# Performance work log

Hardware: AMD Instinct MI355X
Metric: run time of the kernel (lower is better)

Reference implementation:

```python
import jax, jax.numpy as jnp
import numpy as np


def setup_inputs() -> dict:
    key = jax.random.key(0)
    kq, kk, kv = jax.random.split(key, 3)
    B, H, T, D = 2, 8, 8192, 64
    return {
        "Q": jax.random.normal(kq, (B, H, T, D), dtype=jnp.float32),
        "K": jax.random.normal(kk, (B, H, T, D), dtype=jnp.float32),
        "V": jax.random.normal(kv, (B, H, T, D), dtype=jnp.float32),
        "window_size": 512,
    }


def _gather_bands(x, nb, Wn):
    # x: [B,H,T,D] -> [B,H,nb,3*Wn,D], key blocks (i-1, i, i+1) per query block i
    B, H, T, D = x.shape
    xb = x.reshape(B, H, nb, Wn, D)
    xp = jnp.pad(xb, ((0, 0), (0, 0), (1, 1), (0, 0), (0, 0)))
    return jnp.concatenate([xp[:, :, i:i + nb] for i in range(3)], axis=3)


def reference(Q, K, V, window_size):
    # Sliding-window attention: softmax over keys with |q_idx - kv_idx| <= window_size,
    # computed block-sparsely (only the 3 neighboring key blocks per query block).
    B, H, T, D = Q.shape
    Wn = int(window_size)
    assert T % Wn == 0
    nb = T // Wn
    scale = 1.0 / (D ** 0.5)

    Qb = Q.reshape(B, H, nb, Wn, D)
    Kw = _gather_bands(K, nb, Wn)  # [B,H,nb,3W,D]
    Vw = _gather_bands(V, nb, Wn)

    # scores within the band: [B,H,nb,W,3W]
    s = jnp.einsum('bhnqd,bhnkd->bhnqk', Qb, Kw) * scale

    # exact band mask: global q = n*W + q_loc, global kv = (n-1)*W + k_loc
    q_loc = jnp.arange(Wn)[:, None]
    k_loc = jnp.arange(3 * Wn)[None, :]
    band = jnp.abs(q_loc + Wn - k_loc) <= Wn          # [W, 3W]
    kv_g = (jnp.arange(nb)[:, None] - 1) * Wn + jnp.arange(3 * Wn)[None, :]  # [nb, 3W]
    valid = (kv_g >= 0) & (kv_g < T)
    mask = band[None, :, :] & valid[:, None, :]        # [nb, W, 3W]

    s = jnp.where(mask[None, None], s, -jnp.inf)
    p = jax.nn.softmax(s, axis=-1)
    o = jnp.einsum('bhnqk,bhnkd->bhnqd', p, Vw)
    return o.reshape(B, H, T, D)
```

## Files before the change

### kernel.cpp

```cpp
#include <hip/hip_runtime.h>
#include <hip/hip_bf16.h>
#include <stdint.h>

typedef __attribute__((ext_vector_type(8))) short bf16x8;
typedef __attribute__((ext_vector_type(4))) short bf16x4;
typedef __attribute__((ext_vector_type(4))) float f32x4;

#define T_SEQ   8192
#define D_HEAD  64
#define NHEADS  16
#define WIN     512
#define BQ      128
#define BK      64
#define NTILES  (T_SEQ / BK)
#define LDSR    72
#define MASKVAL (-1.0e6f)

#define WS_NEEDED ((size_t)2 * NHEADS * T_SEQ * D_HEAD * 2)

#define MFMA16(a,b,c) __builtin_amdgcn_mfma_f32_16x16x16bf16_1k(a,b,c,0,0,0)

extern "C" __device__ __attribute__((const)) float __ocml_native_exp2_f32(float);
__device__ __forceinline__ float fexp2(float x) { return __ocml_native_exp2_f32(x); }

__device__ __forceinline__ short f2bf(float f) {
    union { float f; uint32_t u; } v; v.f = f;
    return (short)((v.u + 0x7FFFu + ((v.u >> 16) & 1u)) >> 16);
}

__device__ __forceinline__ uint32_t pkbf2(float lo, float hi) {
    union { __hip_bfloat162 h; uint32_t u; } c;
    c.h = __float22bfloat162_rn(make_float2(lo, hi));
    return c.u;
}

__global__ __launch_bounds__(256, 2)
void prep_kv(const float* __restrict__ Kg, const float* __restrict__ Vg,
             short* __restrict__ Kb, short* __restrict__ Vt)
{
    __shared__ float vt[64 * 65];
    const int tid  = threadIdx.x;
    const int tile = blockIdx.x & (NTILES - 1);
    const int head = blockIdx.x >> 7;
    const size_t off = ((size_t)head * T_SEQ + (size_t)tile * BK) * D_HEAD;

    const float* ks = Kg + off;
    short* kd = Kb + off;
    #pragma unroll
    for (int i = 0; i < 4; ++i) {
        int idx = tid + 256 * i;
        float4 v = *(const float4*)(ks + idx * 4);
        short4 h = { f2bf(v.x), f2bf(v.y), f2bf(v.z), f2bf(v.w) };
        *(short4*)(kd + idx * 4) = h;
    }

    const float* vs = Vg + off;
    #pragma unroll
    for (int i = 0; i < 4; ++i) {
        int idx = tid + 256 * i;
        int row = idx >> 4, c4 = (idx & 15) << 2;
        float4 v = *(const float4*)(vs + row * D_HEAD + c4);
        *(float4*)&vt[row * 65 + c4] = v;
    }
    __syncthreads();
    short* vd = Vt + ((size_t)head * NTILES + tile) * (BK * D_HEAD);
    {
        int d = tid >> 2, kq = (tid & 3) << 4;
        short out[16];
        #pragma unroll
        for (int j = 0; j < 16; ++j) out[j] = f2bf(vt[(kq + j) * 65 + d]);
        *(bf16x8*)(vd + d * BK + kq)     = *(bf16x8*)&out[0];
        *(bf16x8*)(vd + d * BK + kq + 8) = *(bf16x8*)&out[8];
    }
}

__global__ __launch_bounds__(256, 4)
void swa_fwd(const float* __restrict__ Qg, const short* __restrict__ Kb,
             const short* __restrict__ Vt, float* __restrict__ Og)
{
    __shared__ short Ks[BK * LDSR];
    __shared__ short Vs[D_HEAD * LDSR];

    const int tid  = threadIdx.x;
    const int wave = tid >> 6;
    const int lane = tid & 63;
    const int lcol = lane & 15;
    const int quad = lane >> 4;

    const int g    = blockIdx.x;
    const int head = (g >> 3) >> 3;
    const int qt   = ((g & 7) << 3) | ((g >> 3) & 7);
    const int q0   = qt * BQ;
    const int tq   = q0 >> 6;

    const float* Qp = Qg + (size_t)head * T_SEQ * D_HEAD;
    const short* Kp = Kb + (size_t)head * T_SEQ * D_HEAD;
    float*       Op = Og + (size_t)head * T_SEQ * D_HEAD;

    const float qscale = 0.125f * 1.44269504088896340736f;
    const int qrow_w = q0 + wave * 32;

    bf16x8 qf[2][2];
    #pragma unroll
    for (int mt = 0; mt < 2; ++mt) {
        const float* qptr = Qp + (size_t)(qrow_w + mt*16 + lcol) * D_HEAD + quad * 8;
        #pragma unroll
        for (int ks = 0; ks < 2; ++ks) {
            float4 a = *(const float4*)(qptr + ks*32);
            float4 b = *(const float4*)(qptr + ks*32 + 4);
            bf16x8 f;
            f[0]=f2bf(a.x*qscale); f[1]=f2bf(a.y*qscale); f[2]=f2bf(a.z*qscale); f[3]=f2bf(a.w*qscale);
            f[4]=f2bf(b.x*qscale); f[5]=f2bf(b.y*qscale); f[6]=f2bf(b.z*qscale); f[7]=f2bf(b.w*qscale);
            qf[mt][ks] = f;
        }
    }

    f32x4 oacc[2][4];
    float l_run[2];
    const f32x4 zero4 = {0.f, 0.f, 0.f, 0.f};
    #pragma unroll
    for (int mt = 0; mt < 2; ++mt) {
        l_run[mt] = 0.f;
        #pragma unroll
        for (int nt = 0; nt < 4; ++nt) oacc[mt][nt] = zero4;
    }

    int t0 = (q0 - WIN) >> 6;            if (t0 < 0) t0 = 0;
    int t1 = (q0 + BQ - 1 + WIN) >> 6;   if (t1 > NTILES - 1) t1 = NTILES - 1;

    const int srow0 = tid >> 3, sc0 = (tid & 7) << 3;
    const int srow1 = srow0 + 32;

    for (int t = t0; t <= t1; ++t) {
        const short* ksrc = Kp + (size_t)t * BK * D_HEAD;
        const short* vsrc = Vt + ((size_t)head * NTILES + t) * (BK * D_HEAD);
        bf16x8 k0 = *(const bf16x8*)(ksrc + tid * 8);
        bf16x8 k1 = *(const bf16x8*)(ksrc + (tid + 256) * 8);
        bf16x8 v0 = *(const bf16x8*)(vsrc + tid * 8);
        bf16x8 v1 = *(const bf16x8*)(vsrc + (tid + 256) * 8);

        __syncthreads();

        *(bf16x8*)&Ks[srow0 * LDSR + sc0] = k0;
        *(bf16x8*)&Ks[srow1 * LDSR + sc0] = k1;
        *(bf16x8*)&Vs[srow0 * LDSR + sc0] = v0;
        *(bf16x8*)&Vs[srow1 * LDSR + sc0] = v1;

        __syncthreads();

        const bool edge = (t < tq - 6) || (t > tq + 7);

        #pragma unroll
        for (int h = 0; h < 2; ++h) {
            f32x4 sc[2][2];
            #pragma unroll
            for (int j = 0; j < 2; ++j) { sc[j][0] = zero4; sc[j][1] = zero4; }
            #pragma unroll
            for (int ks = 0; ks < 2; ++ks) {
                #pragma unroll
                for (int j = 0; j < 2; ++j) {
                    bf16x8 kf = *(const bf16x8*)&Ks[((2*h+j)*16 + lcol)*LDSR + ks*32 + quad*8];
                    sc[j][0] = __builtin_amdgcn_mfma_f32_16x16x32_bf16(kf, qf[0][ks], sc[j][0], 0,0,0);
                    sc[j][1] = __builtin_amdgcn_mfma_f32_16x16x32_bf16(kf, qf[1][ks], sc[j][1], 0,0,0);
                }
            }

            if (edge) {
                #pragma unroll
                for (int j = 0; j < 2; ++j) {
                    const int kg0 = t*BK + (2*h+j)*16 + quad*4;
                    #pragma unroll
                    for (int mt = 0; mt < 2; ++mt) {
                        const int qg = qrow_w + mt*16 + lcol;
                        #pragma unroll
                        for (int r = 0; r < 4; ++r) {
                            int dq = qg - (kg0 + r);
                            if (dq > WIN || dq < -WIN) sc[j][mt][r] = MASKVAL;
                        }
                    }
                }
            }

            #pragma unroll
            for (int j = 0; j < 2; ++j) {
                const int kt = 2*h + j;
                bf16x4 vf[4];
                #pragma unroll
                for (int nt = 0; nt < 4; ++nt)
                    vf[nt] = *(const bf16x4*)&Vs[(nt*16 + lcol)*LDSR + kt*16 + quad*4];
                #pragma unroll
                for (int mt = 0; mt < 2; ++mt) {
                    float p0 = fexp2(sc[j][mt][0]);
                    float p1 = fexp2(sc[j][mt][1]);
                    float p2 = fexp2(sc[j][mt][2]);
                    float p3 = fexp2(sc[j][mt][3]);
                    l_run[mt] += (p0 + p1) + (p2 + p3);
                    union { int2 i; bf16x4 v; } pf;
                    pf.i = make_int2((int)pkbf2(p0, p1), (int)pkbf2(p2, p3));
                    #pragma unroll
                    for (int nt = 0; nt < 4; ++nt)
                        oacc[mt][nt] = MFMA16(vf[nt], pf.v, oacc[mt][nt]);
                }
            }
        }
    }

    #pragma unroll
    for (int mt = 0; mt < 2; ++mt) {
        float l = l_run[mt];
        l += __shfl_xor(l, 16, 64);
        l += __shfl_xor(l, 32, 64);
        float inv = 1.0f / l;
        const int qg = qrow_w + mt*16 + lcol;
        float* op = Op + (size_t)qg * D_HEAD + quad*4;
        #pragma unroll
        for (int nt = 0; nt < 4; ++nt) {
            float4 o = { oacc[mt][nt][0]*inv, oacc[mt][nt][1]*inv,
                         oacc[mt][nt][2]*inv, oacc[mt][nt][3]*inv };
            *(float4*)(op + nt*16) = o;
        }
    }
}

__global__ __launch_bounds__(256, 4)
void swa_fused_fb(const float* __restrict__ Qg, const float* __restrict__ Kg,
                  const float* __restrict__ Vg, float* __restrict__ Og)
{
    __shared__ short Ks[BK * LDSR];
    __shared__ short Vs[D_HEAD * LDSR];
    __shared__ float Vtmp[BK * 65];

    const int tid  = threadIdx.x;
    const int wave = tid >> 6;
    const int lane = tid & 63;
    const int lcol = lane & 15;
    const int quad = lane >> 4;

    const int g    = blockIdx.x;
    const int head = g >> 6;
    const int qt   = ((g & 7) << 3) | ((g >> 3) & 7);
    const int q0   = qt * BQ;
    const int tq   = q0 >> 6;

    const size_t hoff = (size_t)head * T_SEQ * D_HEAD;
    const float* Qp = Qg + hoff;
    const float* Kp = Kg + hoff;
    const float* Vp = Vg + hoff;
    float*       Op = Og + hoff;

    const float qscale = 0.125f * 1.44269504088896340736f;
    const int qrow_w = q0 + wave * 32;

    bf16x8 qf[2][2];
    #pragma unroll
    for (int mt = 0; mt < 2; ++mt) {
        const float* qptr = Qp + (size_t)(qrow_w + mt*16 + lcol) * D_HEAD + quad * 8;
        #pragma unroll
        for (int ks = 0; ks < 2; ++ks) {
            float4 a = *(const float4*)(qptr + ks*32);
            float4 b = *(const float4*)(qptr + ks*32 + 4);
            bf16x8 f;
            f[0]=f2bf(a.x*qscale); f[1]=f2bf(a.y*qscale); f[2]=f2bf(a.z*qscale); f[3]=f2bf(a.w*qscale);
            f[4]=f2bf(b.x*qscale); f[5]=f2bf(b.y*qscale); f[6]=f2bf(b.z*qscale); f[7]=f2bf(b.w*qscale);
            qf[mt][ks] = f;
        }
    }

    f32x4 oacc[2][4];
    float l_run[2];
    const f32x4 zero4 = {0.f, 0.f, 0.f, 0.f};
    #pragma unroll
    for (int mt = 0; mt < 2; ++mt) {
        l_run[mt] = 0.f;
        #pragma unroll
        for (int nt = 0; nt < 4; ++nt) oacc[mt][nt] = zero4;
    }

    int t0 = (q0 - WIN) >> 6;            if (t0 < 0) t0 = 0;
    int t1 = (q0 + BQ - 1 + WIN) >> 6;   if (t1 > NTILES - 1) t1 = NTILES - 1;

    const int krow0 = tid >> 3, kc = (tid & 7) << 3;
    const int krow1 = krow0 + 32;
    const int vrow  = tid >> 4, vc = (tid & 15) << 2;
    const int td    = tid >> 2, tkq = (tid & 3) << 4;

    for (int t = t0; t <= t1; ++t) {
        const float* ksrc = Kp + (size_t)t * BK * D_HEAD;
        const float* vsrc = Vp + (size_t)t * BK * D_HEAD;
        float4 k00 = *(const float4*)(ksrc + krow0*D_HEAD + kc);
        float4 k01 = *(const float4*)(ksrc + krow0*D_HEAD + kc + 4);
        float4 k10 = *(const float4*)(ksrc + krow1*D_HEAD + kc);
        float4 k11 = *(const float4*)(ksrc + krow1*D_HEAD + kc + 4);
        float4 v0  = *(const float4*)(vsrc + (vrow     )*D_HEAD + vc);
        float4 v1  = *(const float4*)(vsrc + (vrow + 16)*D_HEAD + vc);
        float4 v2  = *(const float4*)(vsrc + (vrow + 32)*D_HEAD + vc);
        float4 v3  = *(const float4*)(vsrc + (vrow + 48)*D_HEAD + vc);

        __syncthreads();

        *(float4*)&Vtmp[(vrow     )*65 + vc] = v0;
        *(float4*)&Vtmp[(vrow + 16)*65 + vc] = v1;
        *(float4*)&Vtmp[(vrow + 32)*65 + vc] = v2;
        *(float4*)&Vtmp[(vrow + 48)*65 + vc] = v3;
        *(int4*)&Ks[krow0*LDSR + kc] = make_int4((int)pkbf2(k00.x,k00.y), (int)pkbf2(k00.z,k00.w),
                                                 (int)pkbf2(k01.x,k01.y), (int)pkbf2(k01.z,k01.w));
        *(int4*)&Ks[krow1*LDSR + kc] = make_int4((int)pkbf2(k10.x,k10.y), (int)pkbf2(k10.z,k10.w),
                                                 (int)pkbf2(k11.x,k11.y), (int)pkbf2(k11.z,k11.w));

        __syncthreads();

        {
            uint32_t w0 = pkbf2(Vtmp[(tkq+ 0)*65 + td], Vtmp[(tkq+ 1)*65 + td]);
            uint32_t w1 = pkbf2(Vtmp[(tkq+ 2)*65 + td], Vtmp[(tkq+ 3)*65 + td]);
            uint32_t w2 = pkbf2(Vtmp[(tkq+ 4)*65 + td], Vtmp[(tkq+ 5)*65 + td]);
            uint32_t w3 = pkbf2(Vtmp[(tkq+ 6)*65 + td], Vtmp[(tkq+ 7)*65 + td]);
            uint32_t w4 = pkbf2(Vtmp[(tkq+ 8)*65 + td], Vtmp[(tkq+ 9)*65 + td]);
            uint32_t w5 = pkbf2(Vtmp[(tkq+10)*65 + td], Vtmp[(tkq+11)*65 + td]);
            uint32_t w6 = pkbf2(Vtmp[(tkq+12)*65 + td], Vtmp[(tkq+13)*65 + td]);
            uint32_t w7 = pkbf2(Vtmp[(tkq+14)*65 + td], Vtmp[(tkq+15)*65 + td]);
            *(int4*)&Vs[td*LDSR + tkq]     = make_int4((int)w0,(int)w1,(int)w2,(int)w3);
            *(int4*)&Vs[td*LDSR + tkq + 8] = make_int4((int)w4,(int)w5,(int)w6,(int)w7);
        }

        __syncthreads();

        const bool edge = (t < tq - 6) || (t > tq + 7);

        #pragma unroll
        for (int h = 0; h < 2; ++h) {
            f32x4 sc[2][2];
            #pragma unroll
            for (int j = 0; j < 2; ++j) { sc[j][0] = zero4; sc[j][1] = zero4; }
            #pragma unroll
            for (int ks = 0; ks < 2; ++ks) {
                #pragma unroll
                for (int j = 0; j < 2; ++j) {
                    bf16x8 kf = *(const bf16x8*)&Ks[((2*h+j)*16 + lcol)*LDSR + ks*32 + quad*8];
                    sc[j][0] = __builtin_amdgcn_mfma_f32_16x16x32_bf16(kf, qf[0][ks], sc[j][0], 0,0,0);
                    sc[j][1] = __builtin_amdgcn_mfma_f32_16x16x32_bf16(kf, qf[1][ks], sc[j][1], 0,0,0);
                }
            }

            if (edge) {
                #pragma unroll
                for (int j = 0; j < 2; ++j) {
                    const int kg0 = t*BK + (2*h+j)*16 + quad*4;
                    #pragma unroll
                    for (int mt = 0; mt < 2; ++mt) {
                        const int qg = qrow_w + mt*16 + lcol;
                        #pragma unroll
                        for (int r = 0; r < 4; ++r) {
                            int dq = qg - (kg0 + r);
                            if (dq > WIN || dq < -WIN) sc[j][mt][r] = MASKVAL;
                        }
                    }
                }
            }

            #pragma unroll
            for (int j = 0; j < 2; ++j) {
                const int kt = 2*h + j;
                bf16x4 vf[4];
                #pragma unroll
                for (int nt = 0; nt < 4; ++nt)
                    vf[nt] = *(const bf16x4*)&Vs[(nt*16 + lcol)*LDSR + kt*16 + quad*4];
                #pragma unroll
                for (int mt = 0; mt < 2; ++mt) {
                    float p0 = fexp2(sc[j][mt][0]);
                    float p1 = fexp2(sc[j][mt][1]);
                    float p2 = fexp2(sc[j][mt][2]);
                    float p3 = fexp2(sc[j][mt][3]);
                    l_run[mt] += (p0 + p1) + (p2 + p3);
                    union { int2 i; bf16x4 v; } pf;
                    pf.i = make_int2((int)pkbf2(p0, p1), (int)pkbf2(p2, p3));
                    #pragma unroll
                    for (int nt = 0; nt < 4; ++nt)
                        oacc[mt][nt] = MFMA16(vf[nt], pf.v, oacc[mt][nt]);
                }
            }
        }
    }

    #pragma unroll
    for (int mt = 0; mt < 2; ++mt) {
        float l = l_run[mt];
        l += __shfl_xor(l, 16, 64);
        l += __shfl_xor(l, 32, 64);
        float inv = 1.0f / l;
        const int qg = qrow_w + mt*16 + lcol;
        float* op = Op + (size_t)qg * D_HEAD + quad*4;
        #pragma unroll
        for (int nt = 0; nt < 4; ++nt) {
            float4 o = { oacc[mt][nt][0]*inv, oacc[mt][nt][1]*inv,
                         oacc[mt][nt][2]*inv, oacc[mt][nt][3]*inv };
            *(float4*)(op + nt*16) = o;
        }
    }
}

extern "C" void kernel_launch(void* const* d_in, const int* in_sizes, int n_in,
                              void* d_out, int out_size, void* d_ws, size_t ws_size,
                              hipStream_t stream)
{
    const float* Q = (const float*)d_in[0];
    const float* K = (const float*)d_in[1];
    const float* V = (const float*)d_in[2];
    float* O = (float*)d_out;

    if (ws_size >= WS_NEEDED) {
        short* Kb = (short*)d_ws;
        short* Vt = Kb + (size_t)NHEADS * T_SEQ * D_HEAD;
        prep_kv<<<dim3(NHEADS * NTILES), dim3(256), 0, stream>>>(K, V, Kb, Vt);
        swa_fwd<<<dim3(NHEADS * (T_SEQ / BQ)), dim3(256), 0, stream>>>(Q, Kb, Vt, O);
    } else {
        swa_fused_fb<<<dim3(NHEADS * (T_SEQ / BQ)), dim3(256), 0, stream>>>(Q, K, V, O);
    }
}
```

Measured before the change: 181.0 us.

## Shrink query block to 64 rows per workgroup and double occupancy

The main attention kernel now gives each workgroup 64 query rows, one 16-row MFMA tile per wave instead of two. The grid doubles to 2048 workgroups, launch bounds allow 8 per CU, and the block-to-head mapping is re-swizzled across 8 groups. The aim is more parallelism and occupancy on the many CUs. In exchange each workgroup loads 17 K/V tiles for 64 queries rather than 18 for 128, so global/LDS traffic per query roughly doubles, and the K/V loads are amortized over only one MFMA M-tile per wave.

```diff
diff --git a/kernel.cpp b/kernel.cpp
--- a/kernel.cpp
+++ b/kernel.cpp
@@ -10,7 +10,6 @@
 #define D_HEAD  64
 #define NHEADS  16
 #define WIN     512
-#define BQ      128
 #define BK      64
 #define NTILES  (T_SEQ / BK)
 #define LDSR    72
@@ -74,7 +73,7 @@
     }
 }
 
-__global__ __launch_bounds__(256, 4)
+__global__ __launch_bounds__(256, 8)
 void swa_fwd(const float* __restrict__ Qg, const short* __restrict__ Kb,
              const short* __restrict__ Vt, float* __restrict__ Og)
 {
@@ -88,14 +87,153 @@
     const int quad = lane >> 4;
 
     const int g    = blockIdx.x;
-    const int head = (g >> 3) >> 3;
-    const int qt   = ((g & 7) << 3) | ((g >> 3) & 7);
-    const int q0   = qt * BQ;
-    const int tq   = q0 >> 6;
+    const int wid  = ((g & 7) << 8) | (g >> 3);
+    const int head = wid >> 7;
+    const int qt   = wid & 127;
+    const int q0   = qt * 64;
+    const int tq   = qt;
 
     const float* Qp = Qg + (size_t)head * T_SEQ * D_HEAD;
     const short* Kp = Kb + (size_t)head * T_SEQ * D_HEAD;
     float*       Op = Og + (size_t)head * T_SEQ * D_HEAD;
+
+    const float qscale = 0.125f * 1.44269504088896340736f;
+    const int qrow_w = q0 + wave * 16;
+
+    bf16x8 qf[2];
+    {
+        const float* qptr = Qp + (size_t)(qrow_w + lcol) * D_HEAD + quad * 8;
+        #pragma unroll
+        for (int ks = 0; ks < 2; ++ks) {
+            float4 a = *(const float4*)(qptr + ks*32);
+            float4 b = *(const float4*)(qptr + ks*32 + 4);
+            bf16x8 f;
+            f[0]=f2bf(a.x*qscale); f[1]=f2bf(a.y*qscale); f[2]=f2bf(a.z*qscale); f[3]=f2bf(a.w*qscale);
+            f[4]=f2bf(b.x*qscale); f[5]=f2bf(b.y*qscale); f[6]=f2bf(b.z*qscale); f[7]=f2bf(b.w*qscale);
+            qf[ks] = f;
+        }
+    }
+
+    f32x4 oacc[4];
+    float l_run = 0.f;
+    const f32x4 zero4 = {0.f, 0.f, 0.f, 0.f};
+    #pragma unroll
+    for (int nt = 0; nt < 4; ++nt) oacc[nt] = zero4;
+
+    int t0 = (q0 - WIN) >> 6;            if (t0 < 0) t0 = 0;
+    int t1 = (q0 + 63 + WIN) >> 6;       if (t1 > NTILES - 1) t1 = NTILES - 1;
+
+    const int srow0 = tid >> 3, sc0 = (tid & 7) << 3;
+    const int srow1 = srow0 + 32;
+
+    for (int t = t0; t <= t1; ++t) {
+        const short* ksrc = Kp + (size_t)t * BK * D_HEAD;
+        const short* vsrc = Vt + ((size_t)head * NTILES + t) * (BK * D_HEAD);
+        bf16x8 k0 = *(const bf16x8*)(ksrc + tid * 8);
+        bf16x8 k1 = *(const bf16x8*)(ksrc + (tid + 256) * 8);
+        bf16x8 v0 = *(const bf16x8*)(vsrc + tid * 8);
+        bf16x8 v1 = *(const bf16x8*)(vsrc + (tid + 256) * 8);
+
+        __syncthreads();
+
+        *(bf16x8*)&Ks[srow0 * LDSR + sc0] = k0;
+        *(bf16x8*)&Ks[srow1 * LDSR + sc0] = k1;
+        *(bf16x8*)&Vs[srow0 * LDSR + sc0] = v0;
+        *(bf16x8*)&Vs[srow1 * LDSR + sc0] = v1;
+
+        __syncthreads();
+
+        const bool edge = (t < tq - 7) || (t > tq + 7);
+
+        #pragma unroll
+        for (int h = 0; h < 2; ++h) {
+            f32x4 sc[2];
+            sc[0] = zero4; sc[1] = zero4;
+            #pragma unroll
+            for (int ks = 0; ks < 2; ++ks) {
+                #pragma unroll
+                for (int j = 0; j < 2; ++j) {
+                    bf16x8 kf = *(const bf16x8*)&Ks[((2*h+j)*16 + lcol)*LDSR + ks*32 + quad*8];
+                    sc[j] = __builtin_amdgcn_mfma_f32_16x16x32_bf16(kf, qf[ks], sc[j], 0,0,0);
+                }
+            }
+
+            if (edge) {
+                #pragma unroll
+                for (int j = 0; j < 2; ++j) {
+                    const int kg0 = t*BK + (2*h+j)*16 + quad*4;
+                    const int qg  = qrow_w + lcol;
+                    #pragma unroll
+                    for (int r = 0; r < 4; ++r) {
+                        int dq = qg - (kg0 + r);
+                        if (dq > WIN || dq < -WIN) sc[j][r] = MASKVAL;
+                    }
+                }
+            }
+
+            #pragma unroll
+            for (int j = 0; j < 2; ++j) {
+                const int kt = 2*h + j;
+                bf16x4 vf[4];
+                #pragma unroll
+                for (int nt = 0; nt < 4; ++nt)
+                    vf[nt] = *(const bf16x4*)&Vs[(nt*16 + lcol)*LDSR + kt*16 + quad*4];
+                float p0 = fexp2(sc[j][0]);
+                float p1 = fexp2(sc[j][1]);
+                float p2 = fexp2(sc[j][2]);
+                float p3 = fexp2(sc[j][3]);
+                l_run += (p0 + p1) + (p2 + p3);
+                union { int2 i; bf16x4 v; } pf;
+                pf.i = make_int2((int)pkbf2(p0, p1), (int)pkbf2(p2, p3));
+                #pragma unroll
+                for (int nt = 0; nt < 4; ++nt)
+                    oacc[nt] = MFMA16(vf[nt], pf.v, oacc[nt]);
+            }
+        }
+    }
+
+    {
+        float l = l_run;
+        l += __shfl_xor(l, 16, 64);
+        l += __shfl_xor(l, 32, 64);
+        float inv = 1.0f / l;
+        const int qg = qrow_w + lcol;
+        float* op = Op + (size_t)qg * D_HEAD + quad*4;
+        #pragma unroll
+        for (int nt = 0; nt < 4; ++nt) {
+            float4 o = { oacc[nt][0]*inv, oacc[nt][1]*inv,
+                         oacc[nt][2]*inv, oacc[nt][3]*inv };
+            *(float4*)(op + nt*16) = o;
+        }
+    }
+}
+
+#define BQF     128
+__global__ __launch_bounds__(256, 4)
+void swa_fused_fb(const float* __restrict__ Qg, const float* __restrict__ Kg,
+                  const float* __restrict__ Vg, float* __restrict__ Og)
+{
+    __shared__ short Ks[BK * LDSR];
+    __shared__ short Vs[D_HEAD * LDSR];
+    __shared__ float Vtmp[BK * 65];
+
+    const int tid  = threadIdx.x;
+    const int wave = tid >> 6;
+    const int lane = tid & 63;
+    const int lcol = lane & 15;
+    const int quad = lane >> 4;
+
+    const int g    = blockIdx.x;
+    const int head = g >> 6;
+    const int qt   = ((g & 7) << 3) | ((g >> 3) & 7);
+    const int q0   = qt * BQF;
+    const int tq   = q0 >> 6;
+
+    const size_t hoff = (size_t)head * T_SEQ * D_HEAD;
+    const float* Qp = Qg + hoff;
+    const float* Kp = Kg + hoff;
+    const float* Vp = Vg + hoff;
+    float*       Op = Og + hoff;
 
     const float qscale = 0.125f * 1.44269504088896340736f;
     const int qrow_w = q0 + wave * 32;
@@ -126,25 +264,50 @@
     }
 
     int t0 = (q0 - WIN) >> 6;            if (t0 < 0) t0 = 0;
-    int t1 = (q0 + BQ - 1 + WIN) >> 6;   if (t1 > NTILES - 1) t1 = NTILES - 1;
-
-    const int srow0 = tid >> 3, sc0 = (tid & 7) << 3;
-    const int srow1 = srow0 + 32;
+    int t1 = (q0 + BQF - 1 + WIN) >> 6;  if (t1 > NTILES - 1) t1 = NTILES - 1;
+
+    const int krow0 = tid >> 3, kc = (tid & 7) << 3;
+    const int krow1 = krow0 + 32;
+    const int vrow  = tid >> 4, vc = (tid & 15) << 2;
+    const int td    = tid >> 2, tkq = (tid & 3) << 4;
 
     for (int t = t0; t <= t1; ++t) {
-        const short* ksrc = Kp + (size_t)t * BK * D_HEAD;
-        const short* vsrc = Vt + ((size_t)head * NTILES + t) * (BK * D_HEAD);
-        bf16x8 k0 = *(const bf16x8*)(ksrc + tid * 8);
-        bf16x8 k1 = *(const bf16x8*)(ksrc + (tid + 256) * 8);
-        bf16x8 v0 = *(const bf16x8*)(vsrc + tid * 8);
-        bf16x8 v1 = *(const bf16x8*)(vsrc + (tid + 256) * 8);
+        const float* ksrc = Kp + (size_t)t * BK * D_HEAD;
+        const float* vsrc = Vp + (size_t)t * BK * D_HEAD;
+        float4 k00 = *(const float4*)(ksrc + krow0*D_HEAD + kc);
+        float4 k01 = *(const float4*)(ksrc + krow0*D_HEAD + kc + 4);
+        float4 k10 = *(const float4*)(ksrc + krow1*D_HEAD + kc);
+        float4 k11 = *(const float4*)(ksrc + krow1*D_HEAD + kc + 4);
+        float4 v0  = *(const float4*)(vsrc + (vrow     )*D_HEAD + vc);
+        float4 v1  = *(const float4*)(vsrc + (vrow + 16)*D_HEAD + vc);
+        float4 v2  = *(const float4*)(vsrc + (vrow + 32)*D_HEAD + vc);
+        float4 v3  = *(const float4*)(vsrc + (vrow + 48)*D_HEAD + vc);
 
         __syncthreads();
 
-        *(bf16x8*)&Ks[srow0 * LDSR + sc0] = k0;
-        *(bf16x8*)&Ks[srow1 * LDSR + sc0] = k1;
-        *(bf16x8*)&Vs[srow0 * LDSR + sc0] = v0;
-        *(bf16x8*)&Vs[srow1 * LDSR + sc0] = v1;
+        *(float4*)&Vtmp[(vrow     )*65 + vc] = v0;
+        *(float4*)&Vtmp[(vrow + 16)*65 + vc] = v1;
+        *(float4*)&Vtmp[(vrow + 32)*65 + vc] = v2;
+        *(float4*)&Vtmp[(vrow + 48)*65 + vc] = v3;
+        *(int4*)&Ks[krow0*LDSR + kc] = make_int4((int)pkbf2(k00.x,k00.y), (int)pkbf2(k00.z,k00.w),
+                                                 (int)pkbf2(k01.x,k01.y), (int)pkbf2(k01.z,k01.w));
+        *(int4*)&Ks[krow1*LDSR + kc] = make_int4((int)pkbf2(k10.x,k10.y), (int)pkbf2(k10.z,k10.w),
+                                                 (int)pkbf2(k11.x,k11.y), (int)pkbf2(k11.z,k11.w));
+
+        __syncthreads();
+
+        {
+            uint32_t w0 = pkbf2(Vtmp[(tkq+ 0)*65 + td], Vtmp[(tkq+ 1)*65 + td]);
+            uint32_t w1 = pkbf2(Vtmp[(tkq+ 2)*65 + td], Vtmp[(tkq+ 3)*65 + td]);
+            uint32_t w2 = pkbf2(Vtmp[(tkq+ 4)*65 + td], Vtmp[(tkq+ 5)*65 + td]);
+            uint32_t w3 = pkbf2(Vtmp[(tkq+ 6)*65 + td], Vtmp[(tkq+ 7)*65 + td]);
+            uint32_t w4 = pkbf2(Vtmp[(tkq+ 8)*65 + td], Vtmp[(tkq+ 9)*65 + td]);
+            uint32_t w5 = pkbf2(Vtmp[(tkq+10)*65 + td], Vtmp[(tkq+11)*65 + td]);
+            uint32_t w6 = pkbf2(Vtmp[(tkq+12)*65 + td], Vtmp[(tkq+13)*65 + td]);
+            uint32_t w7 = pkbf2(Vtmp[(tkq+14)*65 + td], Vtmp[(tkq+15)*65 + td]);
+            *(int4*)&Vs[td*LDSR + tkq]     = make_int4((int)w0,(int)w1,(int)w2,(int)w3);
+            *(int4*)&Vs[td*LDSR + tkq + 8] = make_int4((int)w4,(int)w5,(int)w6,(int)w7);
+        }
 
         __syncthreads();
 
@@ -222,182 +385,6 @@
     }
 }
 
-__global__ __launch_bounds__(256, 4)
-void swa_fused_fb(const float* __restrict__ Qg, const float* __restrict__ Kg,
-                  const float* __restrict__ Vg, float* __restrict__ Og)
-{
-    __shared__ short Ks[BK * LDSR];
-    __shared__ short Vs[D_HEAD * LDSR];
-    __shared__ float Vtmp[BK * 65];
-
-    const int tid  = threadIdx.x;
-    const int wave = tid >> 6;
-    const int lane = tid & 63;
-    const int lcol = lane & 15;
-    const int quad = lane >> 4;
-
-    const int g    = blockIdx.x;
-    const int head = g >> 6;
-    const int qt   = ((g & 7) << 3) | ((g >> 3) & 7);
-    const int q0   = qt * BQ;
-    const int tq   = q0 >> 6;
-
-    const size_t hoff = (size_t)head * T_SEQ * D_HEAD;
-    const float* Qp = Qg + hoff;
-    const float* Kp = Kg + hoff;
-    const float* Vp = Vg + hoff;
-    float*       Op = Og + hoff;
-
-    const float qscale = 0.125f * 1.44269504088896340736f;
-    const int qrow_w = q0 + wave * 32;
-
-    bf16x8 qf[2][2];
-    #pragma unroll
-    for (int mt = 0; mt < 2; ++mt) {
-        const float* qptr = Qp + (size_t)(qrow_w + mt*16 + lcol) * D_HEAD + quad * 8;
-        #pragma unroll
-        for (int ks = 0; ks < 2; ++ks) {
-            float4 a = *(const float4*)(qptr + ks*32);
-            float4 b = *(const float4*)(qptr + ks*32 + 4);
-            bf16x8 f;
-            f[0]=f2bf(a.x*qscale); f[1]=f2bf(a.y*qscale); f[2]=f2bf(a.z*qscale); f[3]=f2bf(a.w*qscale);
-            f[4]=f2bf(b.x*qscale); f[5]=f2bf(b.y*qscale); f[6]=f2bf(b.z*qscale); f[7]=f2bf(b.w*qscale);
-            qf[mt][ks] = f;
-        }
-    }
-
-    f32x4 oacc[2][4];
-    float l_run[2];
-    const f32x4 zero4 = {0.f, 0.f, 0.f, 0.f};
-    #pragma unroll
-    for (int mt = 0; mt < 2; ++mt) {
-        l_run[mt] = 0.f;
-        #pragma unroll
-        for (int nt = 0; nt < 4; ++nt) oacc[mt][nt] = zero4;
-    }
-
-    int t0 = (q0 - WIN) >> 6;            if (t0 < 0) t0 = 0;
-    int t1 = (q0 + BQ - 1 + WIN) >> 6;   if (t1 > NTILES - 1) t1 = NTILES - 1;
-
-    const int krow0 = tid >> 3, kc = (tid & 7) << 3;
-    const int krow1 = krow0 + 32;
-    const int vrow  = tid >> 4, vc = (tid & 15) << 2;
-    const int td    = tid >> 2, tkq = (tid & 3) << 4;
-
-    for (int t = t0; t <= t1; ++t) {
-        const float* ksrc = Kp + (size_t)t * BK * D_HEAD;
-        const float* vsrc = Vp + (size_t)t * BK * D_HEAD;
-        float4 k00 = *(const float4*)(ksrc + krow0*D_HEAD + kc);
-        float4 k01 = *(const float4*)(ksrc + krow0*D_HEAD + kc + 4);
-        float4 k10 = *(const float4*)(ksrc + krow1*D_HEAD + kc);
-        float4 k11 = *(const float4*)(ksrc + krow1*D_HEAD + kc + 4);
-        float4 v0  = *(const float4*)(vsrc + (vrow     )*D_HEAD + vc);
-        float4 v1  = *(const float4*)(vsrc + (vrow + 16)*D_HEAD + vc);
-        float4 v2  = *(const float4*)(vsrc + (vrow + 32)*D_HEAD + vc);
-        float4 v3  = *(const float4*)(vsrc + (vrow + 48)*D_HEAD + vc);
-
-        __syncthreads();
-
-        *(float4*)&Vtmp[(vrow     )*65 + vc] = v0;
-        *(float4*)&Vtmp[(vrow + 16)*65 + vc] = v1;
-        *(float4*)&Vtmp[(vrow + 32)*65 + vc] = v2;
-        *(float4*)&Vtmp[(vrow + 48)*65 + vc] = v3;
-        *(int4*)&Ks[krow0*LDSR + kc] = make_int4((int)pkbf2(k00.x,k00.y), (int)pkbf2(k00.z,k00.w),
-                                                 (int)pkbf2(k01.x,k01.y), (int)pkbf2(k01.z,k01.w));
-        *(int4*)&Ks[krow1*LDSR + kc] = make_int4((int)pkbf2(k10.x,k10.y), (int)pkbf2(k10.z,k10.w),
-                                                 (int)pkbf2(k11.x,k11.y), (int)pkbf2(k11.z,k11.w));
-
-        __syncthreads();
-
-        {
-            uint32_t w0 = pkbf2(Vtmp[(tkq+ 0)*65 + td], Vtmp[(tkq+ 1)*65 + td]);
-            uint32_t w1 = pkbf2(Vtmp[(tkq+ 2)*65 + td], Vtmp[(tkq+ 3)*65 + td]);
-            uint32_t w2 = pkbf2(Vtmp[(tkq+ 4)*65 + td], Vtmp[(tkq+ 5)*65 + td]);
-            uint32_t w3 = pkbf2(Vtmp[(tkq+ 6)*65 + td], Vtmp[(tkq+ 7)*65 + td]);
-            uint32_t w4 = pkbf2(Vtmp[(tkq+ 8)*65 + td], Vtmp[(tkq+ 9)*65 + td]);
-            uint32_t w5 = pkbf2(Vtmp[(tkq+10)*65 + td], Vtmp[(tkq+11)*65 + td]);
-            uint32_t w6 = pkbf2(Vtmp[(tkq+12)*65 + td], Vtmp[(tkq+13)*65 + td]);
-            uint32_t w7 = pkbf2(Vtmp[(tkq+14)*65 + td], Vtmp[(tkq+15)*65 + td]);
-            *(int4*)&Vs[td*LDSR + tkq]     = make_int4((int)w0,(int)w1,(int)w2,(int)w3);
-            *(int4*)&Vs[td*LDSR + tkq + 8] = make_int4((int)w4,(int)w5,(int)w6,(int)w7);
-        }
-
-        __syncthreads();
-
-        const bool edge = (t < tq - 6) || (t > tq + 7);
-
-        #pragma unroll
-        for (int h = 0; h < 2; ++h) {
-            f32x4 sc[2][2];
-            #pragma unroll
-            for (int j = 0; j < 2; ++j) { sc[j][0] = zero4; sc[j][1] = zero4; }
-            #pragma unroll
-            for (int ks = 0; ks < 2; ++ks) {
-                #pragma unroll
-                for (int j = 0; j < 2; ++j) {
-                    bf16x8 kf = *(const bf16x8*)&Ks[((2*h+j)*16 + lcol)*LDSR + ks*32 + quad*8];
-                    sc[j][0] = __builtin_amdgcn_mfma_f32_16x16x32_bf16(kf, qf[0][ks], sc[j][0], 0,0,0);
-                    sc[j][1] = __builtin_amdgcn_mfma_f32_16x16x32_bf16(kf, qf[1][ks], sc[j][1], 0,0,0);
-                }
-            }
-
-            if (edge) {
-                #pragma unroll
-                for (int j = 0; j < 2; ++j) {
-                    const int kg0 = t*BK + (2*h+j)*16 + quad*4;
-                    #pragma unroll
-                    for (int mt = 0; mt < 2; ++mt) {
-                        const int qg = qrow_w + mt*16 + lcol;
-                        #pragma unroll
-                        for (int r = 0; r < 4; ++r) {
-                            int dq = qg - (kg0 + r);
-                            if (dq > WIN || dq < -WIN) sc[j][mt][r] = MASKVAL;
-                        }
-                    }
-                }
-            }
-
-            #pragma unroll
-            for (int j = 0; j < 2; ++j) {
-                const int kt = 2*h + j;
-                bf16x4 vf[4];
-                #pragma unroll
-                for (int nt = 0; nt < 4; ++nt)
-                    vf[nt] = *(const bf16x4*)&Vs[(nt*16 + lcol)*LDSR + kt*16 + quad*4];
-                #pragma unroll
-                for (int mt = 0; mt < 2; ++mt) {
-                    float p0 = fexp2(sc[j][mt][0]);
-                    float p1 = fexp2(sc[j][mt][1]);
-                    float p2 = fexp2(sc[j][mt][2]);
-                    float p3 = fexp2(sc[j][mt][3]);
-                    l_run[mt] += (p0 + p1) + (p2 + p3);
-                    union { int2 i; bf16x4 v; } pf;
-                    pf.i = make_int2((int)pkbf2(p0, p1), (int)pkbf2(p2, p3));
-                    #pragma unroll
-                    for (int nt = 0; nt < 4; ++nt)
-                        oacc[mt][nt] = MFMA16(vf[nt], pf.v, oacc[mt][nt]);
-                }
-            }
-        }
-    }
-
-    #pragma unroll
-    for (int mt = 0; mt < 2; ++mt) {
-        float l = l_run[mt];
-        l += __shfl_xor(l, 16, 64);
-        l += __shfl_xor(l, 32, 64);
-        float inv = 1.0f / l;
-        const int qg = qrow_w + mt*16 + lcol;
-        float* op = Op + (size_t)qg * D_HEAD + quad*4;
-        #pragma unroll
-        for (int nt = 0; nt < 4; ++nt) {
-            float4 o = { oacc[mt][nt][0]*inv, oacc[mt][nt][1]*inv,
-                         oacc[mt][nt][2]*inv, oacc[mt][nt][3]*inv };
-            *(float4*)(op + nt*16) = o;
-        }
-    }
-}
-
 extern "C" void kernel_launch(void* const* d_in, const int* in_sizes, int n_in,
                               void* d_out, int out_size, void* d_ws, size_t ws_size,
                               hipStream_t stream)
@@ -411,8 +398,8 @@
         short* Kb = (short*)d_ws;
         short* Vt = Kb + (size_t)NHEADS * T_SEQ * D_HEAD;
         prep_kv<<<dim3(NHEADS * NTILES), dim3(256), 0, stream>>>(K, V, Kb, Vt);
-        swa_fwd<<<dim3(NHEADS * (T_SEQ / BQ)), dim3(256), 0, stream>>>(Q, Kb, Vt, O);
+        swa_fwd<<<dim3(NHEADS * (T_SEQ / 64)), dim3(256), 0, stream>>>(Q, Kb, Vt, O);
     } else {
-        swa_fused_fb<<<dim3(NHEADS * (T_SEQ / BQ)), dim3(256), 0, stream>>>(Q, K, V, O);
-    }
-}
+        swa_fused_fb<<<dim3(NHEADS * (T_SEQ / BQF)), dim3(256), 0, stream>>>(Q, K, V, O);
+    }
+}
```

Result: slower. 197.4 us (+9.1%).

## Double-buffer K/V tiles in LDS with register prefetch two tiles ahead

Applied to the files above, without the earlier changes.

The main attention kernel now uses two LDS buffers for K and V. The next tile is written into the alternate buffer while the current one is computed, and the global loads for the tile after that are issued early. This replaces two barriers per iteration with one and hides global load latency behind the MFMA work. LDS use doubles, which may reduce occupancy, and the fallback kernel only gets renamed symbols.

```diff
diff --git a/kernel.cpp b/kernel.cpp
--- a/kernel.cpp
+++ b/kernel.cpp
@@ -78,8 +78,8 @@
 void swa_fwd(const float* __restrict__ Qg, const short* __restrict__ Kb,
              const short* __restrict__ Vt, float* __restrict__ Og)
 {
-    __shared__ short Ks[BK * LDSR];
-    __shared__ short Vs[D_HEAD * LDSR];
+    __shared__ short Ks[2][BK * LDSR];
+    __shared__ short Vs[2][BK * LDSR];
 
     const int tid  = threadIdx.x;
     const int wave = tid >> 6;
@@ -88,7 +88,7 @@
     const int quad = lane >> 4;
 
     const int g    = blockIdx.x;
-    const int head = (g >> 3) >> 3;
+    const int head = g >> 6;
     const int qt   = ((g & 7) << 3) | ((g >> 3) & 7);
     const int q0   = qt * BQ;
     const int tq   = q0 >> 6;
@@ -130,24 +130,48 @@
 
     const int srow0 = tid >> 3, sc0 = (tid & 7) << 3;
     const int srow1 = srow0 + 32;
-
+    const int sOff0 = srow0 * LDSR + sc0;
+    const int sOff1 = srow1 * LDSR + sc0;
+
+    {
+        const short* ksrc = Kp + (size_t)t0 * BK * D_HEAD;
+        const short* vsrc = Vt + ((size_t)head * NTILES + t0) * (BK * D_HEAD);
+        *(bf16x8*)&Ks[0][sOff0] = *(const bf16x8*)(ksrc + tid * 8);
+        *(bf16x8*)&Ks[0][sOff1] = *(const bf16x8*)(ksrc + (tid + 256) * 8);
+        *(bf16x8*)&Vs[0][sOff0] = *(const bf16x8*)(vsrc + tid * 8);
+        *(bf16x8*)&Vs[0][sOff1] = *(const bf16x8*)(vsrc + (tid + 256) * 8);
+    }
+    bf16x8 k0, k1, v0, v1;
+    {
+        const int tn = (t0 + 1 <= t1) ? t0 + 1 : t1;
+        const short* ksrc = Kp + (size_t)tn * BK * D_HEAD;
+        const short* vsrc = Vt + ((size_t)head * NTILES + tn) * (BK * D_HEAD);
+        k0 = *(const bf16x8*)(ksrc + tid * 8);
+        k1 = *(const bf16x8*)(ksrc + (tid + 256) * 8);
+        v0 = *(const bf16x8*)(vsrc + tid * 8);
+        v1 = *(const bf16x8*)(vsrc + (tid + 256) * 8);
+    }
+    __syncthreads();
+
+    int p = 0;
     for (int t = t0; t <= t1; ++t) {
-        const short* ksrc = Kp + (size_t)t * BK * D_HEAD;
-        const short* vsrc = Vt + ((size_t)head * NTILES + t) * (BK * D_HEAD);
-        bf16x8 k0 = *(const bf16x8*)(ksrc + tid * 8);
-        bf16x8 k1 = *(const bf16x8*)(ksrc + (tid + 256) * 8);
-        bf16x8 v0 = *(const bf16x8*)(vsrc + tid * 8);
-        bf16x8 v1 = *(const bf16x8*)(vsrc + (tid + 256) * 8);
-
-        __syncthreads();
-
-        *(bf16x8*)&Ks[srow0 * LDSR + sc0] = k0;
-        *(bf16x8*)&Ks[srow1 * LDSR + sc0] = k1;
-        *(bf16x8*)&Vs[srow0 * LDSR + sc0] = v0;
-        *(bf16x8*)&Vs[srow1 * LDSR + sc0] = v1;
-
-        __syncthreads();
-
+        *(bf16x8*)&Ks[p^1][sOff0] = k0;
+        *(bf16x8*)&Ks[p^1][sOff1] = k1;
+        *(bf16x8*)&Vs[p^1][sOff0] = v0;
+        *(bf16x8*)&Vs[p^1][sOff1] = v1;
+
+        {
+            const int tn = (t + 2 <= t1) ? t + 2 : t1;
+            const short* ksrc = Kp + (size_t)tn * BK * D_HEAD;
+            const short* vsrc = Vt + ((size_t)head * NTILES + tn) * (BK * D_HEAD);
+            k0 = *(const bf16x8*)(ksrc + tid * 8);
+            k1 = *(const bf16x8*)(ksrc + (tid + 256) * 8);
+            v0 = *(const bf16x8*)(vsrc + tid * 8);
+            v1 = *(const bf16x8*)(vsrc + (tid + 256) * 8);
+        }
+
+        const short* Kcur = Ks[p];
+        const short* Vcur = Vs[p];
         const bool edge = (t < tq - 6) || (t > tq + 7);
 
         #pragma unroll
@@ -159,7 +183,7 @@
             for (int ks = 0; ks < 2; ++ks) {
                 #pragma unroll
                 for (int j = 0; j < 2; ++j) {
-                    bf16x8 kf = *(const bf16x8*)&Ks[((2*h+j)*16 + lcol)*LDSR + ks*32 + quad*8];
+                    bf16x8 kf = *(const bf16x8*)&Kcur[((2*h+j)*16 + lcol)*LDSR + ks*32 + quad*8];
                     sc[j][0] = __builtin_amdgcn_mfma_f32_16x16x32_bf16(kf, qf[0][ks], sc[j][0], 0,0,0);
                     sc[j][1] = __builtin_amdgcn_mfma_f32_16x16x32_bf16(kf, qf[1][ks], sc[j][1], 0,0,0);
                 }
@@ -187,7 +211,7 @@
                 bf16x4 vf[4];
                 #pragma unroll
                 for (int nt = 0; nt < 4; ++nt)
-                    vf[nt] = *(const bf16x4*)&Vs[(nt*16 + lcol)*LDSR + kt*16 + quad*4];
+                    vf[nt] = *(const bf16x4*)&Vcur[(nt*16 + lcol)*LDSR + kt*16 + quad*4];
                 #pragma unroll
                 for (int mt = 0; mt < 2; ++mt) {
                     float p0 = fexp2(sc[j][mt][0]);
@@ -203,6 +227,9 @@
                 }
             }
         }
+
+        __syncthreads();
+        p ^= 1;
     }
 
     #pragma unroll
@@ -222,12 +249,13 @@
     }
 }
 
+#define BQF     128
 __global__ __launch_bounds__(256, 4)
 void swa_fused_fb(const float* __restrict__ Qg, const float* __restrict__ Kg,
                   const float* __restrict__ Vg, float* __restrict__ Og)
 {
-    __shared__ short Ks[BK * LDSR];
-    __shared__ short Vs[D_HEAD * LDSR];
+    __shared__ short Ksf[BK * LDSR];
+    __shared__ short Vsf[D_HEAD * LDSR];
     __shared__ float Vtmp[BK * 65];
 
     const int tid  = threadIdx.x;
@@ -239,7 +267,7 @@
     const int g    = blockIdx.x;
     const int head = g >> 6;
     const int qt   = ((g & 7) << 3) | ((g >> 3) & 7);
-    const int q0   = qt * BQ;
+    const int q0   = qt * BQF;
     const int tq   = q0 >> 6;
 
     const size_t hoff = (size_t)head * T_SEQ * D_HEAD;
@@ -277,7 +305,7 @@
     }
 
     int t0 = (q0 - WIN) >> 6;            if (t0 < 0) t0 = 0;
-    int t1 = (q0 + BQ - 1 + WIN) >> 6;   if (t1 > NTILES - 1) t1 = NTILES - 1;
+    int t1 = (q0 + BQF - 1 + WIN) >> 6;  if (t1 > NTILES - 1) t1 = NTILES - 1;
 
     const int krow0 = tid >> 3, kc = (tid & 7) << 3;
     const int krow1 = krow0 + 32;
@@ -302,10 +330,10 @@
         *(float4*)&Vtmp[(vrow + 16)*65 + vc] = v1;
         *(float4*)&Vtmp[(vrow + 32)*65 + vc] = v2;
         *(float4*)&Vtmp[(vrow + 48)*65 + vc] = v3;
-        *(int4*)&Ks[krow0*LDSR + kc] = make_int4((int)pkbf2(k00.x,k00.y), (int)pkbf2(k00.z,k00.w),
-                                                 (int)pkbf2(k01.x,k01.y), (int)pkbf2(k01.z,k01.w));
-        *(int4*)&Ks[krow1*LDSR + kc] = make_int4((int)pkbf2(k10.x,k10.y), (int)pkbf2(k10.z,k10.w),
-                                                 (int)pkbf2(k11.x,k11.y), (int)pkbf2(k11.z,k11.w));
+        *(int4*)&Ksf[krow0*LDSR + kc] = make_int4((int)pkbf2(k00.x,k00.y), (int)pkbf2(k00.z,k00.w),
+                                                  (int)pkbf2(k01.x,k01.y), (int)pkbf2(k01.z,k01.w));
+        *(int4*)&Ksf[krow1*LDSR + kc] = make_int4((int)pkbf2(k10.x,k10.y), (int)pkbf2(k10.z,k10.w),
+                                                  (int)pkbf2(k11.x,k11.y), (int)pkbf2(k11.z,k11.w));
 
         __syncthreads();
 
@@ -318,8 +346,8 @@
             uint32_t w5 = pkbf2(Vtmp[(tkq+10)*65 + td], Vtmp[(tkq+11)*65 + td]);
             uint32_t w6 = pkbf2(Vtmp[(tkq+12)*65 + td], Vtmp[(tkq+13)*65 + td]);
             uint32_t w7 = pkbf2(Vtmp[(tkq+14)*65 + td], Vtmp[(tkq+15)*65 + td]);
-            *(int4*)&Vs[td*LDSR + tkq]     = make_int4((int)w0,(int)w1,(int)w2,(int)w3);
-            *(int4*)&Vs[td*LDSR + tkq + 8] = make_int4((int)w4,(int)w5,(int)w6,(int)w7);
+            *(int4*)&Vsf[td*LDSR + tkq]     = make_int4((int)w0,(int)w1,(int)w2,(int)w3);
+            *(int4*)&Vsf[td*LDSR + tkq + 8] = make_int4((int)w4,(int)w5,(int)w6,(int)w7);
         }
 
         __syncthreads();
@@ -335,7 +363,7 @@
             for (int ks = 0; ks < 2; ++ks) {
                 #pragma unroll
                 for (int j = 0; j < 2; ++j) {
-                    bf16x8 kf = *(const bf16x8*)&Ks[((2*h+j)*16 + lcol)*LDSR + ks*32 + quad*8];
+                    bf16x8 kf = *(const bf16x8*)&Ksf[((2*h+j)*16 + lcol)*LDSR + ks*32 + quad*8];
                     sc[j][0] = __builtin_amdgcn_mfma_f32_16x16x32_bf16(kf, qf[0][ks], sc[j][0], 0,0,0);
                     sc[j][1] = __builtin_amdgcn_mfma_f32_16x16x32_bf16(kf, qf[1][ks], sc[j][1], 0,0,0);
                 }
@@ -363,7 +391,7 @@
                 bf16x4 vf[4];
                 #pragma unroll
                 for (int nt = 0; nt < 4; ++nt)
-                    vf[nt] = *(const bf16x4*)&Vs[(nt*16 + lcol)*LDSR + kt*16 + quad*4];
+                    vf[nt] = *(const bf16x4*)&Vsf[(nt*16 + lcol)*LDSR + kt*16 + quad*4];
                 #pragma unroll
                 for (int mt = 0; mt < 2; ++mt) {
                     float p0 = fexp2(sc[j][mt][0]);
@@ -413,6 +441,6 @@
         prep_kv<<<dim3(NHEADS * NTILES), dim3(256), 0, stream>>>(K, V, Kb, Vt);
         swa_fwd<<<dim3(NHEADS * (T_SEQ / BQ)), dim3(256), 0, stream>>>(Q, Kb, Vt, O);
     } else {
-        swa_fused_fb<<<dim3(NHEADS * (T_SEQ / BQ)), dim3(256), 0, stream>>>(Q, K, V, O);
-    }
-}
+        swa_fused_fb<<<dim3(NHEADS * (T_SEQ / BQF)), dim3(256), 0, stream>>>(Q, K, V, O);
+    }
+}
```

Result: slower. 204.5 us (+13.0%).
